# Performance work log

Measured on AMD Instinct MI355X. Metric: run time of the kernel, lower is better.

Reference implementation:

```python
import jax, jax.numpy as jnp
import numpy as np
from jax import lax

NHEAD = 8
DC = 32
BN_EPS = 1e-5


def setup_inputs() -> dict:
    key = jax.random.key(0)
    ks = jax.random.split(key, 8)
    b, t, h, w = 8, 128, 32, 64
    l = h * w
    prev_attn = jax.random.uniform(ks[0], (b * NHEAD, t, l), dtype=jnp.float32)
    curr_attn = jax.random.uniform(ks[1], (b * NHEAD, t, l), dtype=jnp.float32)
    key_padding_mask = jax.random.bernoulli(ks[2], 0.2, (b, l))  # True = padded
    conv_w = jax.random.normal(ks[3], (DC, 2 * NHEAD, 5, 5), dtype=jnp.float32) * 0.05
    conv_b = jnp.zeros((DC,), dtype=jnp.float32)
    proj_w = jax.random.normal(ks[4], (NHEAD, DC, 1, 1), dtype=jnp.float32) * 0.1
    bn_gamma = jnp.ones((NHEAD,), dtype=jnp.float32)
    bn_beta = jnp.zeros((NHEAD,), dtype=jnp.float32)
    return {"prev_attn": prev_attn, "curr_attn": curr_attn,
            "key_padding_mask": key_padding_mask, "h": 32,
            "conv_w": conv_w, "conv_b": conv_b, "proj_w": proj_w,
            "bn_gamma": bn_gamma, "bn_beta": bn_beta}


def _forward(prev_attn, curr_attn, conv_w, conv_b, proj_w, bn_gamma, bn_beta,
             key_padding_mask, h):
    b, l = key_padding_mask.shape
    t = curr_attn.shape[1]
    w = l // h
    n = NHEAD
    prev = prev_attn.reshape(b, n, t, l)
    curr = curr_attn.reshape(b, n, t, l)
    attns = jnp.concatenate([prev, curr], axis=1)            # (b, 2n, t, l)
    attns = jnp.cumsum(attns, axis=2) - attns                # exclusive cumsum over t
    # 'b n t (h w) -> (b t) n h w'
    attns = attns.transpose(0, 2, 1, 3).reshape(b * t, 2 * n, h, w)
    cov = lax.conv_general_dilated(attns, conv_w, (1, 1), [(2, 2), (2, 2)],
                                   dimension_numbers=("NCHW", "OIHW", "NCHW"))
    cov = jax.nn.relu(cov + conv_b[None, :, None, None])
    # mask: 'b (h w) -> (b t) 1 h w'
    mask = jnp.broadcast_to(key_padding_mask.reshape(b, 1, 1, h, w),
                            (b, t, 1, h, w)).reshape(b * t, 1, h, w)
    cov = jnp.where(mask, 0.0, cov)
    # 1x1 conv, no bias
    cov = jnp.einsum("bdhw,nd->bnhw", cov, proj_w[:, :, 0, 0])  # (bt, n, h, w)
    # MaskBatchNorm2d: BN over unmasked pixels (training-mode batch stats)
    nm = (~mask).astype(cov.dtype)                              # (bt, 1, h, w)
    cnt = jnp.maximum(nm.sum(), 1.0)
    mean = (cov * nm).sum(axis=(0, 2, 3)) / cnt                 # (n,)
    diff = cov - mean[None, :, None, None]
    var = (diff * diff * nm).sum(axis=(0, 2, 3)) / cnt          # biased var
    y = bn_gamma[None, :, None, None] * diff * lax.rsqrt(var + BN_EPS)[None, :, None, None] \
        + bn_beta[None, :, None, None]
    cov = jnp.where(mask, cov, y)
    # '(b t) n h w -> (b n) t (h w)'
    cov = cov.reshape(b, t, n, h * w).transpose(0, 2, 1, 3).reshape(b * n, t, h * w)
    return cov


def reference(prev_attn, curr_attn, key_padding_mask, h,
              conv_w, conv_b, proj_w, bn_gamma, bn_beta):
    return _forward(prev_attn, curr_attn, conv_w, conv_b, proj_w,
                    bn_gamma, bn_beta, key_padding_mask, h)
```

## Files before the change

### kernel.cpp

```cpp
#include <hip/hip_runtime.h>
#include <hip/hip_bf16.h>


typedef __attribute__((ext_vector_type(4))) float f32x4;
typedef __attribute__((ext_vector_type(8))) short short8;
typedef __attribute__((ext_vector_type(8))) unsigned short u16x8;

#define B_   8
#define NH   8
#define T_   128
#define H_   32
#define W_   64
#define L_   2048
#define CIN  16
#define DCC  32
#define WSTR 420

__device__ __forceinline__ unsigned short f2h(float f){
  _Float16 h = (_Float16)f;
  return __builtin_bit_cast(unsigned short, h);
}
__device__ __forceinline__ float h2f(unsigned short u){
  _Float16 h = __builtin_bit_cast(_Float16, u);
  return (float)h;
}
__device__ __forceinline__ int swz(int a){ return a ^ ((a >> 3) & 0x30); }

__global__ void k_cumsum(const float* __restrict__ prev,
                         const float* __restrict__ curr,
                         uint2* __restrict__ cum2)
{
  int gid = blockIdx.x * 256 + threadIdx.x;
  int p4 = gid & 511;
  int ci = (gid >> 9) & 15;
  int b  = gid >> 13;
  const float* src = ((ci < 8)
      ? prev + ((size_t)(b*8 + ci) * T_) * L_
      : curr + ((size_t)(b*8 + ci - 8) * T_) * L_) + p4*4;
  uint2* dst = cum2 + ((size_t)(b*CIN + ci) * T_) * (L_/4) + p4;
  float a0 = 0.f, a1 = 0.f, a2 = 0.f, a3 = 0.f;
  for (int t = 0; t < T_; t++){
    uint2 o;
    o.x = (unsigned)f2h(a0) | ((unsigned)f2h(a1) << 16);
    o.y = (unsigned)f2h(a2) | ((unsigned)f2h(a3) << 16);
    dst[(size_t)t * (L_/4)] = o;
    f32x4 v = *(const f32x4*)(src + (size_t)t * L_);
    a0 += v.x; a1 += v.y; a2 += v.z; a3 += v.w;
  }
}

__global__ void k_mask(const void* __restrict__ mraw,
                       unsigned char* __restrict__ mB,
                       float* __restrict__ cntOut)
{
  __shared__ int s_flags;
  __shared__ int s_cnt;
  int tid = threadIdx.x;
  if (tid == 0){ s_flags = 0; s_cnt = 0; }
  __syncthreads();
  const unsigned* w = (const unsigned*)mraw;
  int fl = 0;
  for (int i = tid; i < 4096; i += 256){
    unsigned v = w[i];
    if (v == 0x3F800000u) fl |= 2;
    else if (v > 1u)      fl |= 1;
    else if (v == 1u)     fl |= 4;
  }
  if (fl) atomicOr(&s_flags, fl);
  __syncthreads();
  int flags = s_flags;
  int mode = (flags & 1) ? 0 : ((flags & 2) ? 2 : ((flags & 4) ? 1 : 0));
  int c = 0;
  int base = blockIdx.x * 1024;
  for (int k = 0; k < 4; k++){
    int i = base + k*256 + tid;
    int m;
    if (mode == 0)      m = (((const unsigned char*)mraw)[i] != 0);
    else if (mode == 2) m = (((const float*)mraw)[i] != 0.f);
    else                m = (((const int*)mraw)[i] != 0);
    mB[i] = (unsigned char)m;
    c += 1 - m;
  }
  atomicAdd(&s_cnt, c);
  __syncthreads();
  if (tid == 0) atomicAdd(cntOut, 128.0f * (float)s_cnt);
}

__global__ void k_wprep(const float* __restrict__ convw,
                        const float* __restrict__ projw,
                        unsigned short* __restrict__ Wt,
                        unsigned short* __restrict__ Pt)
{
  int tid = threadIdx.x;
  int co = blockIdx.x;
  if (co < 32){
    for (int k = tid; k < WSTR; k += 256){
      float v = 0.f;
      if (k < 400){
        int tap = k >> 4, ci = k & 15;
        int dy = tap / 5, dx = tap - dy*5;
        v = convw[(((co*CIN + ci)*5 + dy)*5) + dx];
      }
      Wt[co*WSTR + k] = f2h(v);
    }
  } else {
    for (int idx = tid; idx < 16*32; idx += 256){
      int n = idx >> 5, q = idx & 31;
      float v = (n < 8) ? projw[n*32 + 16*(q & 1) + (q >> 1)] : 0.f;
      Pt[idx] = f2h(v);
    }
  }
}

__global__ __launch_bounds__(256, 2) void k_conv(
    const unsigned short* __restrict__ cumIn,
    const unsigned short* __restrict__ Wt,
    const unsigned short* __restrict__ Pt,
    const unsigned char* __restrict__ mB,
    const float* __restrict__ convb,
    unsigned short* __restrict__ cov,
    float* __restrict__ slots)
{
  __shared__ alignas(16) unsigned short img[20*68*16];
  __shared__ alignas(16) unsigned short wlds[DCC*WSTR];
  __shared__ alignas(16) unsigned short plds[16*32];
  __shared__ alignas(16) unsigned sval[4][16*20];
  __shared__ unsigned long long mbl[16];

  const int tid  = threadIdx.x;
  const int bid  = blockIdx.x;
  const int half = bid & 1;
  const int bt   = bid >> 1;
  const int t    = bt & 127;
  const int b    = bt >> 7;
  const int ylo  = half * 16;
  const int lane = tid & 63;
  const int wv   = tid >> 6;
  const int mrow = lane & 15;
  const int kb   = lane >> 4;

  if (wv == 0){
    #pragma unroll
    for (int k2 = 0; k2 < 16; k2++){
      int m = mB[b*L_ + half*1024 + k2*64 + lane];
      unsigned long long bal = __ballot(m != 0);
      if (lane == 0) mbl[k2] = bal;
    }
  }

  {
    const uint4* srcw = (const uint4*)Wt;  uint4* dstw = (uint4*)wlds;
    for (int i = tid; i < (DCC*WSTR*2)/16; i += 256) dstw[i] = srcw[i];
    const uint4* srcp = (const uint4*)Pt;  uint4* dstp = (uint4*)plds;
    for (int i = tid; i < (16*32*2)/16; i += 256) dstp[i] = srcp[i];
  }

  for (int it = tid; it < 640; it += 256){
    int cp  = it & 7;
    int xxi = (it >> 3) & 3;
    int yy  = it >> 5;
    int xx  = (xxi < 2) ? xxi : 64 + xxi;
    int ad  = ((yy*68 + xx)*16 + 2*cp)*2;
    *(unsigned*)((char*)img + swz(ad)) = 0u;
  }
  #pragma unroll
  for (int iter = 0; iter < 5; iter++){
    int it = iter*256 + tid;
    int xc = it & 7;
    int cp = (it >> 3) & 7;
    int yy = it >> 6;
    int y  = ylo - 2 + yy;
    u16x8 v0 = (u16x8)0, v1 = (u16x8)0;
    if (y >= 0 && y < H_){
      const unsigned short* r0 = cumIn + (((size_t)(b*CIN + 2*cp) * T_ + t) * L_) + y*W_ + xc*8;
      v0 = *(const u16x8*)r0;
      v1 = *(const u16x8*)(r0 + (size_t)T_ * L_);
    }
    int sbase = ((yy*68 + 2 + xc*8)*16 + 2*cp)*2;
    #pragma unroll
    for (int j = 0; j < 8; j++){
      unsigned wd = (unsigned)v0[j] | ((unsigned)v1[j] << 16);
      int ad = sbase + j*32;
      *(unsigned*)((char*)img + swz(ad)) = wd;
    }
  }
  __syncthreads();

  const float cb0 = convb[mrow];
  const float cb1 = convb[mrow + 16];
  const short8 pbf = *(const short8*)&plds[mrow*32 + kb*8];
  const int bw = mrow*840 + kb*16;

  int offs_[13];
  #pragma unroll
  for (int ks = 0; ks < 13; ks++){
    int tap = ks*2 + (kb >> 1);
    if (tap > 24) tap = 24;
    int dy = tap / 5, dx = tap - dy*5;
    offs_[ks] = (dy*68 + dx)*32 + (kb & 1)*16;
  }

  float ssum = 0.f, ssq = 0.f;

  #pragma unroll 1
  for (int c = 0; c < 2; c++){
    const int pbase = wv*256 + c*128;
    const unsigned long long mw0 = mbl[(pbase >> 6)];
    const unsigned long long mw1 = mbl[(pbase >> 6) + 1];
    const int base_u = ((pbase >> 6)*68 + mrow)*32;
    f32x4 acc[8][2];
    #pragma unroll
    for (int mt = 0; mt < 8; mt++){ acc[mt][0] = (f32x4)0.f; acc[mt][1] = (f32x4)0.f; }

    #pragma unroll
    for (int ks = 0; ks < 13; ks++){
      short8 bfa = *(const short8*)((const char*)wlds + bw + ks*64);
      short8 bfb = *(const short8*)((const char*)wlds + bw + 13440 + ks*64);
      const char* p0 = (const char*)img + swz(base_u + offs_[ks]);
      const char* p1 = (const char*)img + swz(base_u + 2176 + offs_[ks]);
      short8 a[8];
      a[0] = *(const short8*)(p0);
      a[1] = *(const short8*)(p0 + 512);
      a[2] = *(const short8*)(p0 + 1024);
      a[3] = *(const short8*)(p0 + 1536);
      a[4] = *(const short8*)(p1);
      a[5] = *(const short8*)(p1 + 512);
      a[6] = *(const short8*)(p1 + 1024);
      a[7] = *(const short8*)(p1 + 1536);
      #pragma unroll
      for (int mt = 0; mt < 8; mt++){
        acc[mt][0] = __builtin_amdgcn_mfma_f32_16x16x32_f16(a[mt], bfa, acc[mt][0], 0, 0, 0);
        acc[mt][1] = __builtin_amdgcn_mfma_f32_16x16x32_f16(a[mt], bfb, acc[mt][1], 0, 0, 0);
      }
    }

    unsigned* sv = &sval[wv][0];
    #pragma unroll
    for (int mt = 0; mt <= 8; mt++){
      if (mt >= 1){
        const int m = mt - 1;
        short8 pa = *(const short8*)&sv[mrow*20 + kb*4];
        f32x4 pc = (f32x4)0.f;
        pc = __builtin_amdgcn_mfma_f32_16x16x32_f16(pa, pbf, pc, 0, 0, 0);
        if (mrow < 8){
          const unsigned long long mwm = (m < 4) ? mw0 : mw1;
          size_t covbase = (((size_t)bt*NH + mrow) * L_) + half*1024 + pbase + m*16 + kb*4;
          uint2 st;
          st.x = (unsigned)f2h(pc[0]) | ((unsigned)f2h(pc[1]) << 16);
          st.y = (unsigned)f2h(pc[2]) | ((unsigned)f2h(pc[3]) << 16);
          *(uint2*)&cov[covbase] = st;
          #pragma unroll
          for (int r = 0; r < 4; r++){
            int bi = (m*16 + kb*4 + r) & 63;
            if (!((mwm >> bi) & 1)){ ssum += pc[r]; ssq += pc[r]*pc[r]; }
          }
        }
      }
      if (mt < 8){
        const unsigned long long mw = (mt < 4) ? mw0 : mw1;
        #pragma unroll
        for (int r = 0; r < 4; r++){
          int bi  = (mt*16 + kb*4 + r) & 63;
          int msk = (int)((mw >> bi) & 1);
          float v0 = fmaxf(acc[mt][0][r] + cb0, 0.f);
          float v1 = fmaxf(acc[mt][1][r] + cb1, 0.f);
          if (msk){ v0 = 0.f; v1 = 0.f; }
          unsigned pd = (unsigned)f2h(v0) | ((unsigned)f2h(v1) << 16);
          sv[(kb*4 + r)*20 + mrow] = pd;
        }
      }
    }
  }

  ssum += __shfl_xor(ssum, 16);
  ssum += __shfl_xor(ssum, 32);
  ssq  += __shfl_xor(ssq, 16);
  ssq  += __shfl_xor(ssq, 32);
  if (lane < 8){
    atomicAdd(&slots[(bid & 7)*16 + lane],     ssum);
    atomicAdd(&slots[(bid & 7)*16 + 8 + lane], ssq);
  }
}

__global__ void k_stats(const float* __restrict__ slots,
                        const float* __restrict__ cntp,
                        const float* __restrict__ gamma,
                        const float* __restrict__ beta,
                        float* __restrict__ ab)
{
  int tid = threadIdx.x;
  if (tid < 8){
    double s = 0.0, q = 0.0;
    for (int i = 0; i < 8; i++){
      s += (double)slots[i*16 + tid];
      q += (double)slots[i*16 + 8 + tid];
    }
    double cnt  = (double)fmaxf(*cntp, 1.0f);
    double mean = s / cnt;
    double var  = q / cnt - mean*mean;
    float inv = (float)(1.0 / sqrt(var + 1e-5));
    float A = gamma[tid] * inv;
    float Bc = beta[tid] - (float)mean * A;
    ab[tid]     = A;
    ab[8 + tid] = Bc;
  }
}

__global__ void k_out(const unsigned short* __restrict__ cov,
                      const unsigned char* __restrict__ mB,
                      const float* __restrict__ ab,
                      float* __restrict__ out)
{
  size_t gid = (size_t)blockIdx.x * 256 + threadIdx.x;
  size_t e = gid * 8;
  int px = (int)(e & 2047);
  size_t r = e >> 11;
  int t = (int)(r & 127); r >>= 7;
  int n = (int)(r & 7);
  int b = (int)(r >> 3);
  const unsigned short* cp = cov + ((((size_t)b*T_ + t)*NH + n) << 11) + px;
  u16x8 cv = *(const u16x8*)cp;
  unsigned long long mm = *(const unsigned long long*)(mB + (size_t)b*L_ + px);
  float A = ab[n], Bc = ab[8 + n];
  float res[8];
  #pragma unroll
  for (int j = 0; j < 8; j++){
    float v = h2f(cv[j]);
    res[j] = ((mm >> (8*j)) & 0xFFull) ? v : (A*v + Bc);
  }
  f32x4* o = (f32x4*)(out + e);
  o[0] = (f32x4){res[0], res[1], res[2], res[3]};
  o[1] = (f32x4){res[4], res[5], res[6], res[7]};
}

extern "C" void kernel_launch(void* const* d_in, const int* in_sizes, int n_in,
                              void* d_out, int out_size, void* d_ws, size_t ws_size,
                              hipStream_t stream)
{
  const float* prev  = (const float*)d_in[0];
  const float* curr  = (const float*)d_in[1];
  const void*  mraw  = d_in[2];
  const float* convw = (const float*)d_in[4];
  const float* convb = (const float*)d_in[5];
  const float* projw = (const float*)d_in[6];
  const float* gamma = (const float*)d_in[7];
  const float* beta  = (const float*)d_in[8];
  float* out = (float*)d_out;

  char* ws = (char*)d_ws;
  unsigned short* cumIn = (unsigned short*)(ws);
  unsigned short* cov   = (unsigned short*)(ws + 67108864);
  unsigned char*  mB    = (unsigned char*) (ws + 100663296);
  unsigned short* Wt    = (unsigned short*)(ws + 100679680);
  unsigned short* Pt    = (unsigned short*)(ws + 100706560);
  float* slots          = (float*)(ws + 100707584);
  float* cntp           = (float*)(ws + 100708096);
  float* ab             = (float*)(ws + 100708160);
  if (ws_size < (size_t)100708224) return;

  hipMemsetAsync(slots, 0, 640, stream);
  k_mask  <<<16,   256, 0, stream>>>(mraw, mB, cntp);
  k_wprep <<<33,   256, 0, stream>>>(convw, projw, Wt, Pt);
  k_cumsum<<<256,  256, 0, stream>>>(prev, curr, (uint2*)cumIn);
  k_conv  <<<2048, 256, 0, stream>>>(cumIn, Wt, Pt, mB, convb, cov, slots);
  k_stats <<<1,    64,  0, stream>>>(slots, cntp, gamma, beta, ab);
  k_out   <<<8192, 256, 0, stream>>>(cov, mB, ab, out);
}
```

Baseline: 188.6 us.

## Read conv weights from global, raise occupancy, fuse prep kernels

Removes the per-block LDS copy of the conv weight matrix and loads MFMA B fragments directly from global memory, freeing LDS so launch bounds can allow three blocks per CU. The mask and weight preparation kernels are merged into one launch to save launch overhead, the cumsum loop is unrolled, and the MFMA burst is wrapped with wave priority raising. The trade-off is extra global/L1 traffic and latency for weight fragments inside the inner loop, plus tighter register limits from the higher occupancy target.

```diff
diff --git a/kernel.cpp b/kernel.cpp
--- a/kernel.cpp
+++ b/kernel.cpp
@@ -39,6 +39,7 @@
       : curr + ((size_t)(b*8 + ci - 8) * T_) * L_) + p4*4;
   uint2* dst = cum2 + ((size_t)(b*CIN + ci) * T_) * (L_/4) + p4;
   float a0 = 0.f, a1 = 0.f, a2 = 0.f, a3 = 0.f;
+  #pragma unroll 4
   for (int t = 0; t < T_; t++){
     uint2 o;
     o.x = (unsigned)f2h(a0) | ((unsigned)f2h(a1) << 16);
@@ -49,51 +50,18 @@
   }
 }
 
-__global__ void k_mask(const void* __restrict__ mraw,
+__global__ void k_prep(const float* __restrict__ convw,
+                       const float* __restrict__ projw,
+                       const void* __restrict__ mraw,
+                       unsigned short* __restrict__ Wt,
+                       unsigned short* __restrict__ Pt,
                        unsigned char* __restrict__ mB,
                        float* __restrict__ cntOut)
 {
-  __shared__ int s_flags;
-  __shared__ int s_cnt;
   int tid = threadIdx.x;
-  if (tid == 0){ s_flags = 0; s_cnt = 0; }
-  __syncthreads();
-  const unsigned* w = (const unsigned*)mraw;
-  int fl = 0;
-  for (int i = tid; i < 4096; i += 256){
-    unsigned v = w[i];
-    if (v == 0x3F800000u) fl |= 2;
-    else if (v > 1u)      fl |= 1;
-    else if (v == 1u)     fl |= 4;
-  }
-  if (fl) atomicOr(&s_flags, fl);
-  __syncthreads();
-  int flags = s_flags;
-  int mode = (flags & 1) ? 0 : ((flags & 2) ? 2 : ((flags & 4) ? 1 : 0));
-  int c = 0;
-  int base = blockIdx.x * 1024;
-  for (int k = 0; k < 4; k++){
-    int i = base + k*256 + tid;
-    int m;
-    if (mode == 0)      m = (((const unsigned char*)mraw)[i] != 0);
-    else if (mode == 2) m = (((const float*)mraw)[i] != 0.f);
-    else                m = (((const int*)mraw)[i] != 0);
-    mB[i] = (unsigned char)m;
-    c += 1 - m;
-  }
-  atomicAdd(&s_cnt, c);
-  __syncthreads();
-  if (tid == 0) atomicAdd(cntOut, 128.0f * (float)s_cnt);
-}
-
-__global__ void k_wprep(const float* __restrict__ convw,
-                        const float* __restrict__ projw,
-                        unsigned short* __restrict__ Wt,
-                        unsigned short* __restrict__ Pt)
-{
-  int tid = threadIdx.x;
-  int co = blockIdx.x;
-  if (co < 32){
+  int blk = blockIdx.x;
+  if (blk < 32){
+    int co = blk;
     for (int k = tid; k < WSTR; k += 256){
       float v = 0.f;
       if (k < 400){
@@ -103,16 +71,47 @@
       }
       Wt[co*WSTR + k] = f2h(v);
     }
-  } else {
+  } else if (blk == 32){
     for (int idx = tid; idx < 16*32; idx += 256){
       int n = idx >> 5, q = idx & 31;
       float v = (n < 8) ? projw[n*32 + 16*(q & 1) + (q >> 1)] : 0.f;
       Pt[idx] = f2h(v);
     }
-  }
-}
-
-__global__ __launch_bounds__(256, 2) void k_conv(
+  } else {
+    __shared__ int s_flags;
+    __shared__ int s_cnt;
+    if (tid == 0){ s_flags = 0; s_cnt = 0; }
+    __syncthreads();
+    const unsigned* w = (const unsigned*)mraw;
+    int fl = 0;
+    for (int i = tid; i < 4096; i += 256){
+      unsigned v = w[i];
+      if (v == 0x3F800000u) fl |= 2;
+      else if (v > 1u)      fl |= 1;
+      else if (v == 1u)     fl |= 4;
+    }
+    if (fl) atomicOr(&s_flags, fl);
+    __syncthreads();
+    int flags = s_flags;
+    int mode = (flags & 1) ? 0 : ((flags & 2) ? 2 : ((flags & 4) ? 1 : 0));
+    int c = 0;
+    int base = (blk - 33) * 1024;
+    for (int k = 0; k < 4; k++){
+      int i = base + k*256 + tid;
+      int m;
+      if (mode == 0)      m = (((const unsigned char*)mraw)[i] != 0);
+      else if (mode == 2) m = (((const float*)mraw)[i] != 0.f);
+      else                m = (((const int*)mraw)[i] != 0);
+      mB[i] = (unsigned char)m;
+      c += 1 - m;
+    }
+    atomicAdd(&s_cnt, c);
+    __syncthreads();
+    if (tid == 0) atomicAdd(cntOut, 128.0f * (float)s_cnt);
+  }
+}
+
+__global__ __launch_bounds__(256, 3) void k_conv(
     const unsigned short* __restrict__ cumIn,
     const unsigned short* __restrict__ Wt,
     const unsigned short* __restrict__ Pt,
@@ -122,7 +121,6 @@
     float* __restrict__ slots)
 {
   __shared__ alignas(16) unsigned short img[20*68*16];
-  __shared__ alignas(16) unsigned short wlds[DCC*WSTR];
   __shared__ alignas(16) unsigned short plds[16*32];
   __shared__ alignas(16) unsigned sval[4][16*20];
   __shared__ unsigned long long mbl[16];
@@ -146,13 +144,10 @@
       unsigned long long bal = __ballot(m != 0);
       if (lane == 0) mbl[k2] = bal;
     }
-  }
-
-  {
-    const uint4* srcw = (const uint4*)Wt;  uint4* dstw = (uint4*)wlds;
-    for (int i = tid; i < (DCC*WSTR*2)/16; i += 256) dstw[i] = srcw[i];
-    const uint4* srcp = (const uint4*)Pt;  uint4* dstp = (uint4*)plds;
-    for (int i = tid; i < (16*32*2)/16; i += 256) dstp[i] = srcp[i];
+  } else if (wv == 1){
+    const uint4* srcp = (const uint4*)Pt;
+    uint4* dstp = (uint4*)plds;
+    if (lane < 64) { for (int i = lane; i < 64; i += 64) dstp[i] = srcp[i]; }
   }
 
   for (int it = tid; it < 640; it += 256){
@@ -189,7 +184,7 @@
   const float cb0 = convb[mrow];
   const float cb1 = convb[mrow + 16];
   const short8 pbf = *(const short8*)&plds[mrow*32 + kb*8];
-  const int bw = mrow*840 + kb*16;
+  const unsigned short* Wg = Wt + mrow*WSTR + kb*8;
 
   int offs_[13];
   #pragma unroll
@@ -204,6 +199,8 @@
 
   #pragma unroll 1
   for (int c = 0; c < 2; c++){
+    int wofs = 0;
+    asm volatile("" : "+v"(wofs));
     const int pbase = wv*256 + c*128;
     const unsigned long long mw0 = mbl[(pbase >> 6)];
     const unsigned long long mw1 = mbl[(pbase >> 6) + 1];
@@ -214,8 +211,8 @@
 
     #pragma unroll
     for (int ks = 0; ks < 13; ks++){
-      short8 bfa = *(const short8*)((const char*)wlds + bw + ks*64);
-      short8 bfb = *(const short8*)((const char*)wlds + bw + 13440 + ks*64);
+      short8 bfa = *(const short8*)(Wg + wofs + ks*32);
+      short8 bfb = *(const short8*)(Wg + wofs + 6720 + ks*32);
       const char* p0 = (const char*)img + swz(base_u + offs_[ks]);
       const char* p1 = (const char*)img + swz(base_u + 2176 + offs_[ks]);
       short8 a[8];
@@ -227,11 +224,13 @@
       a[5] = *(const short8*)(p1 + 512);
       a[6] = *(const short8*)(p1 + 1024);
       a[7] = *(const short8*)(p1 + 1536);
+      __builtin_amdgcn_s_setprio(1);
       #pragma unroll
       for (int mt = 0; mt < 8; mt++){
         acc[mt][0] = __builtin_amdgcn_mfma_f32_16x16x32_f16(a[mt], bfa, acc[mt][0], 0, 0, 0);
         acc[mt][1] = __builtin_amdgcn_mfma_f32_16x16x32_f16(a[mt], bfb, acc[mt][1], 0, 0, 0);
       }
+      __builtin_amdgcn_s_setprio(0);
     }
 
     unsigned* sv = &sval[wv][0];
@@ -359,8 +358,7 @@
   if (ws_size < (size_t)100708224) return;
 
   hipMemsetAsync(slots, 0, 640, stream);
-  k_mask  <<<16,   256, 0, stream>>>(mraw, mB, cntp);
-  k_wprep <<<33,   256, 0, stream>>>(convw, projw, Wt, Pt);
+  k_prep  <<<49,   256, 0, stream>>>(convw, projw, mraw, Wt, Pt, mB, cntp);
   k_cumsum<<<256,  256, 0, stream>>>(prev, curr, (uint2*)cumIn);
   k_conv  <<<2048, 256, 0, stream>>>(cumIn, Wt, Pt, mB, convb, cov, slots);
   k_stats <<<1,    64,  0, stream>>>(slots, cntp, gamma, beta, ab);
```

New measurement: 179.6 us. 4.7% less time.
